# Optimization experiments

Hardware: AMD Instinct MI355X
Metric: run time of the kernel (lower is better)

Reference implementation:

```python
import jax, jax.numpy as jnp
import numpy as np

E, E2, T, C, H = 500_000, 1_000_000, 1_000_000, 64, 64
EPS, EPS2 = 0.0, 0.0  # train_eps=False, eps=eps2=0.0


def setup_inputs() -> dict:
    key = jax.random.key(0)
    ks = jax.random.split(key, 16)
    s = 1.0 / np.sqrt(C)
    return {
        "edge_attr": jax.random.normal(ks[0], (E, C), jnp.float32),
        "edge_attr2": jax.random.normal(ks[1], (E2, C), jnp.float32),
        # 6 projection layers (C -> C)
        "Wp": jax.random.normal(ks[2], (6, C, C), jnp.float32) * s,
        "bp": jnp.zeros((6, C), jnp.float32),
        # MLP 0 (for 1-hop edges): C -> H -> C
        "W1a": jax.random.normal(ks[3], (C, H), jnp.float32) * s,
        "b1a": jnp.zeros((H,), jnp.float32),
        "W2a": jax.random.normal(ks[4], (H, C), jnp.float32) * (1.0 / np.sqrt(H)),
        "b2a": jnp.zeros((C,), jnp.float32),
        # MLP 1 (for 2-hop edges): C -> H -> C
        "W1b": jax.random.normal(ks[5], (C, H), jnp.float32) * s,
        "b1b": jnp.zeros((H,), jnp.float32),
        "W2b": jax.random.normal(ks[6], (H, C), jnp.float32) * (1.0 / np.sqrt(H)),
        "b2b": jnp.zeros((C,), jnp.float32),
        # triangle index lists [3, T]; all values < E so valid for both edge arrays
        "triangle_1_1_1": jax.random.randint(ks[7], (3, T), 0, E, jnp.int64),
        "triangle_1_1_2": jax.random.randint(ks[8], (3, T), 0, E, jnp.int64),
        "triangle_1_2_2": jax.random.randint(ks[9], (3, T), 0, E, jnp.int64),
        "triangle_2_2_2": jax.random.randint(ks[10], (3, T), 0, E, jnp.int64),
        "inverse_edge_1": jax.random.randint(ks[11], (E,), 0, E, jnp.int64),
        "inverse_edge_2": jax.random.randint(ks[12], (E2,), 0, E, jnp.int64),
    }


def reference(edge_attr, edge_attr2, Wp, bp, W1a, b1a, W2a, b2a,
              W1b, b1b, W2b, b2b,
              triangle_1_1_1, triangle_1_1_2, triangle_1_2_2, triangle_2_2_2,
              inverse_edge_1, inverse_edge_2):
    num_edges = edge_attr.shape[0]
    num_edges2 = edge_attr2.shape[0]

    def proj(i, x):  # Linear proj i applied to gathered-sum features
        return x @ Wp[i] + bp[i]

    def mlp_a(x):
        return jax.nn.relu(x @ W1a + b1a) @ W2a + b2a

    def mlp_b(x):
        return jax.nn.relu(x @ W1b + b1b) @ W2b + b2b

    ij111, ik111, kj111 = triangle_1_1_1
    ij112, ik112, kj112 = triangle_1_1_2
    ij122, ik122, kj122 = triangle_1_2_2
    ij222, ik222, kj222 = triangle_2_2_2

    m111 = jax.ops.segment_sum(proj(0, edge_attr[ik111] + edge_attr[kj111]), ij111, num_segments=num_edges)
    m112 = jax.ops.segment_sum(proj(1, edge_attr[ik112] + edge_attr2[kj112]), ij112, num_segments=num_edges)
    m122 = jax.ops.segment_sum(proj(2, edge_attr2[ik122] + edge_attr2[kj122]), ij122, num_segments=num_edges)
    edge_attr = mlp_a(edge_attr * (1.0 + EPS) + m111 + m112 + m112[inverse_edge_1] + m122)

    m211 = jax.ops.segment_sum(proj(3, edge_attr[ij112] + edge_attr[ik112]), kj112, num_segments=num_edges2)
    m212 = jax.ops.segment_sum(proj(4, edge_attr[ij122] + edge_attr2[kj122]), ik122, num_segments=num_edges2)
    m222 = jax.ops.segment_sum(proj(5, edge_attr2[ik222] + edge_attr2[kj222]), ij222, num_segments=num_edges2)
    edge_attr2 = mlp_b(edge_attr2 * (1.0 + EPS2) + m211 + m212 + m212[inverse_edge_2] + m222)

    return (edge_attr, edge_attr2)
```

## Files before the change

kernel.cpp:

```cpp
#include <hip/hip_runtime.h>

#define CH 64
typedef unsigned int uint;
typedef unsigned short ushort;

typedef __attribute__((ext_vector_type(8))) short bf16x8;
typedef __attribute__((ext_vector_type(4))) float f32x4;

__device__ __forceinline__ float bf_lo(uint u){ union{uint a;float f;}c; c.a=u<<16; return c.f; }
__device__ __forceinline__ float bf_hi(uint u){ union{uint a;float f;}c; c.a=u&0xffff0000u; return c.f; }
__device__ __forceinline__ ushort f2bf(float f){
    uint a = __float_as_uint(f);
    a = (a + 0x7fffu + ((a>>16)&1u)) >> 16;
    return (ushort)a;
}
__device__ __forceinline__ uint pack2(float lo, float hi){
    return (uint)f2bf(lo) | ((uint)f2bf(hi) << 16);
}
__device__ __forceinline__ void atom_pk(uint* addr, float lo, float hi){
    uint v = pack2(lo, hi);
    asm volatile("global_atomic_pk_add_bf16 %0, %1, off" :: "v"(addr), "v"(v) : "memory");
}

template<bool ABF, bool BBF>
__global__ __launch_bounds__(256) void scatter_sum(
    const void* __restrict__ Av, const void* __restrict__ Bv,
    const int* __restrict__ idx_dst, const int* __restrict__ idx_a,
    const int* __restrict__ idx_b, int T,
    uint* __restrict__ S, float* __restrict__ cnt)
{
    const int l32  = threadIdx.x & 31;
    const int half = (threadIdx.x >> 5) & 1;
    const int wave  = blockIdx.x * (blockDim.x >> 6) + (threadIdx.x >> 6);
    const int nwave = gridDim.x * (blockDim.x >> 6);
    for (int w = wave; 2 * w < T; w += nwave) {
        const int t = 2 * w + half;
        if (t >= T) continue;
        const int ia = idx_a[t], ib = idx_b[t], id = idx_dst[t];
        float ax, ay, bx, by;
        if (ABF) { uint u = ((const uint*)Av)[(size_t)ia*32 + l32]; ax = bf_lo(u); ay = bf_hi(u); }
        else     { float2 v = ((const float2*)Av)[(size_t)ia*32 + l32]; ax = v.x; ay = v.y; }
        if (BBF) { uint u = ((const uint*)Bv)[(size_t)ib*32 + l32]; bx = bf_lo(u); by = bf_hi(u); }
        else     { float2 v = ((const float2*)Bv)[(size_t)ib*32 + l32]; bx = v.x; by = v.y; }
        atom_pk(S + (size_t)id*32 + l32, ax+bx, ay+by);
        if (l32 == 0) atomicAdd(&cnt[id], 1.0f);
    }
}

__global__ __launch_bounds__(256) void conv_bf16_kernel(
    const float* __restrict__ src, uint* __restrict__ dst, long n4)
{
    long i = (long)blockIdx.x * blockDim.x + threadIdx.x;
    const long stride = (long)gridDim.x * blockDim.x;
    for (; i < n4; i += stride) {
        const float4 v = ((const float4*)src)[i];
        uint2 o; o.x = pack2(v.x, v.y); o.y = pack2(v.z, v.w);
        ((uint2*)dst)[i] = o;
    }
}

__global__ __launch_bounds__(256) void fused_finalize_mfma(
    const float* __restrict__ base,
    const uint* __restrict__ SA, const float* __restrict__ cA,
    const float* __restrict__ WA, const float* __restrict__ bA,
    const uint* __restrict__ SB, const float* __restrict__ cB,
    const float* __restrict__ WB, const float* __restrict__ bB,
    const uint* __restrict__ SC, const float* __restrict__ cC,
    const float* __restrict__ WC, const float* __restrict__ bC,
    const int* __restrict__ inv,
    const float* __restrict__ W1, const float* __restrict__ b1,
    const float* __restrict__ W2, const float* __restrict__ b2,
    int N, float* __restrict__ out)
{
    __shared__ __attribute__((aligned(16))) char lds[49152];
    const int tid = threadIdx.x;

    const float* Wlist[5] = {WA, WB, WC, W1, W2};
    #pragma unroll
    for (int m = 0; m < 5; ++m) {
        const float* Wm = Wlist[m];
        for (int idx = tid; idx < 4096; idx += 256) {
            const int k = idx >> 6, col = idx & 63;
            *(ushort*)(lds + m*8192 + col*128 + ((2*k) ^ ((col&7)<<4))) = f2bf(Wm[idx]);
        }
    }
    __syncthreads();

    const int w = tid >> 6, lane = tid & 63;
    const int ln = lane & 15, grp = lane >> 4;
    const int r0 = blockIdx.x * 64 + w * 16;
    const int ra = (r0 + ln) < N ? (r0 + ln) : (N - 1);
    const int iva = inv[ra];
    char* zl = lds + 40960 + w * 2048;

    auto ldS = [&](const uint* Srow, int kc) {
        union { uint4 u; bf16x8 h; } c;
        c.u = *(const uint4*)(Srow + kc*16 + grp*4);
        return c.h;
    };
    auto ldS2 = [&](const uint* r1, const uint* r2, int kc) {
        const uint4 a = *(const uint4*)(r1 + kc*16 + grp*4);
        const uint4 b = *(const uint4*)(r2 + kc*16 + grp*4);
        union { uint4 u; bf16x8 h; } c;
        c.u.x = pack2(bf_lo(a.x)+bf_lo(b.x), bf_hi(a.x)+bf_hi(b.x));
        c.u.y = pack2(bf_lo(a.y)+bf_lo(b.y), bf_hi(a.y)+bf_hi(b.y));
        c.u.z = pack2(bf_lo(a.z)+bf_lo(b.z), bf_hi(a.z)+bf_hi(b.z));
        c.u.w = pack2(bf_lo(a.w)+bf_lo(b.w), bf_hi(a.w)+bf_hi(b.w));
        return c.h;
    };
    auto ldW = [&](int m, int kc, int ct) {
        const int col = ct*16 + ln;
        const int k2  = (kc*32 + grp*8) * 2;
        return *(const bf16x8*)(lds + m*8192 + col*128 + (k2 ^ ((col&7)<<4)));
    };
    auto ldZ = [&](int kc) {
        const int k2 = (kc*32 + grp*8) * 2;
        return *(const bf16x8*)(zl + ln*128 + (k2 ^ ((ln&7)<<4)));
    };
    auto stZ = [&](int row, int col, float v) {
        *(ushort*)(zl + row*128 + ((2*col) ^ ((row&7)<<4))) = f2bf(v);
    };

    const uint* SArow  = SA + (size_t)ra * 32;
    const uint* SBrow  = SB + (size_t)ra * 32;
    const uint* SCrow  = SC + (size_t)ra * 32;
    const uint* SCrow2 = SC + (size_t)iva * 32;

    const f32x4 z4 = {0.f, 0.f, 0.f, 0.f};
    f32x4 acc[4] = {z4, z4, z4, z4};

    #pragma unroll
    for (int kc = 0; kc < 2; ++kc) {
        const bf16x8 aA = ldS(SArow, kc);
        const bf16x8 aB = ldS(SBrow, kc);
        const bf16x8 aC = ldS2(SCrow, SCrow2, kc);
        #pragma unroll
        for (int ct = 0; ct < 4; ++ct) {
            acc[ct] = __builtin_amdgcn_mfma_f32_16x16x32_bf16(aA, ldW(0,kc,ct), acc[ct], 0,0,0);
            acc[ct] = __builtin_amdgcn_mfma_f32_16x16x32_bf16(aB, ldW(1,kc,ct), acc[ct], 0,0,0);
            acc[ct] = __builtin_amdgcn_mfma_f32_16x16x32_bf16(aC, ldW(2,kc,ct), acc[ct], 0,0,0);
        }
    }

    #pragma unroll
    for (int reg = 0; reg < 4; ++reg) {
        const int rd = r0 + grp*4 + reg;
        const int rc = rd < N ? rd : (N - 1);
        const float fA = cA[rc], fB = cB[rc];
        const float fC = cC[rc] + cC[inv[rc]];
        #pragma unroll
        for (int ct = 0; ct < 4; ++ct) {
            const int col = ct*16 + ln;
            acc[ct][reg] += base[(size_t)rc*64 + col] + fA*bA[col] + fB*bB[col] + fC*bC[col];
        }
    }
    #pragma unroll
    for (int ct = 0; ct < 4; ++ct)
        #pragma unroll
        for (int reg = 0; reg < 4; ++reg)
            stZ(grp*4 + reg, ct*16 + ln, acc[ct][reg]);

    f32x4 hacc[4] = {z4, z4, z4, z4};
    #pragma unroll
    for (int kc = 0; kc < 2; ++kc) {
        const bf16x8 az = ldZ(kc);
        #pragma unroll
        for (int ct = 0; ct < 4; ++ct)
            hacc[ct] = __builtin_amdgcn_mfma_f32_16x16x32_bf16(az, ldW(3,kc,ct), hacc[ct], 0,0,0);
    }
    #pragma unroll
    for (int ct = 0; ct < 4; ++ct)
        #pragma unroll
        for (int reg = 0; reg < 4; ++reg)
            stZ(grp*4 + reg, ct*16 + ln, fmaxf(hacc[ct][reg] + b1[ct*16 + ln], 0.f));

    f32x4 oacc[4] = {z4, z4, z4, z4};
    #pragma unroll
    for (int kc = 0; kc < 2; ++kc) {
        const bf16x8 ah = ldZ(kc);
        #pragma unroll
        for (int ct = 0; ct < 4; ++ct)
            oacc[ct] = __builtin_amdgcn_mfma_f32_16x16x32_bf16(ah, ldW(4,kc,ct), oacc[ct], 0,0,0);
    }
    #pragma unroll
    for (int reg = 0; reg < 4; ++reg) {
        const int rd = r0 + grp*4 + reg;
        if (rd < N) {
            #pragma unroll
            for (int ct = 0; ct < 4; ++ct) {
                const int col = ct*16 + ln;
                out[(size_t)rd*64 + col] = oacc[ct][reg] + b2[col];
            }
        }
    }
}

extern "C" void kernel_launch(void* const* d_in, const int* in_sizes, int n_in,
                              void* d_out, int out_size, void* d_ws, size_t ws_size,
                              hipStream_t stream)
{
    const float* ea  = (const float*)d_in[0];
    const float* ea2 = (const float*)d_in[1];
    const float* Wp  = (const float*)d_in[2];
    const float* bp  = (const float*)d_in[3];
    const float* W1a = (const float*)d_in[4];
    const float* b1a = (const float*)d_in[5];
    const float* W2a = (const float*)d_in[6];
    const float* b2a = (const float*)d_in[7];
    const float* W1b = (const float*)d_in[8];
    const float* b1b = (const float*)d_in[9];
    const float* W2b = (const float*)d_in[10];
    const float* b2b = (const float*)d_in[11];
    const int* t111 = (const int*)d_in[12];
    const int* t112 = (const int*)d_in[13];
    const int* t122 = (const int*)d_in[14];
    const int* t222 = (const int*)d_in[15];
    const int* inv1 = (const int*)d_in[16];
    const int* inv2 = (const int*)d_in[17];

    const int E    = in_sizes[0] / CH;
    const int E2   = in_sizes[1] / CH;
    const int T111 = in_sizes[12] / 3;
    const int T112 = in_sizes[13] / 3;
    const int T122 = in_sizes[14] / 3;
    const int T222 = in_sizes[15] / 3;

    float* out1 = (float*)d_out;
    float* out2 = out1 + (size_t)E * CH;

    const size_t R = (size_t)(E > E2 ? E : E2);
    char* p = (char*)d_ws;
    uint*  SA = (uint*)p;  p += R * 128;
    uint*  SB = (uint*)p;  p += R * 128;
    uint*  SC = (uint*)p;  p += R * 128;
    float* cA = (float*)p; p += R * 4;
    float* cB = (float*)p; p += R * 4;
    float* cC = (float*)p; p += R * 4;
    size_t used = (size_t)(p - (char*)d_ws);
    uint* ea2_bf = nullptr;
    uint* ea_bf  = nullptr;
    if (ws_size >= used + (size_t)E2 * 128) { ea2_bf = (uint*)p; p += (size_t)E2 * 128; used += (size_t)E2 * 128; }
    if (ws_size >= used + (size_t)E  * 128) { ea_bf  = (uint*)p; }

    const dim3 blk256(256);
    const int SCAT_NB = 4096;

    auto scat = [&](const void* A, bool abf, const void* B, bool bbf,
                    const int* dst, const int* ia, const int* ib, int T,
                    uint* S, float* c) {
        if (abf && bbf)
            scatter_sum<true, true ><<<SCAT_NB, blk256, 0, stream>>>(A, B, dst, ia, ib, T, S, c);
        else if (abf)
            scatter_sum<true, false><<<SCAT_NB, blk256, 0, stream>>>(A, B, dst, ia, ib, T, S, c);
        else if (bbf)
            scatter_sum<false, true><<<SCAT_NB, blk256, 0, stream>>>(A, B, dst, ia, ib, T, S, c);
        else
            scatter_sum<false, false><<<SCAT_NB, blk256, 0, stream>>>(A, B, dst, ia, ib, T, S, c);
    };

    if (ea2_bf) conv_bf16_kernel<<<2048, blk256, 0, stream>>>(ea2, ea2_bf, (long)E2 * 16);
    if (ea_bf)  conv_bf16_kernel<<<2048, blk256, 0, stream>>>(ea,  ea_bf,  (long)E  * 16);

    const void* eaS  = ea_bf  ? (const void*)ea_bf  : (const void*)ea;
    const void* ea2S = ea2_bf ? (const void*)ea2_bf : (const void*)ea2;
    const bool eaB = ea_bf != nullptr, ea2B = ea2_bf != nullptr;

    hipMemsetAsync(SA, 0, (size_t)E * 128, stream);
    hipMemsetAsync(SB, 0, (size_t)E * 128, stream);
    hipMemsetAsync(SC, 0, (size_t)E * 128, stream);
    hipMemsetAsync(cA, 0, (size_t)E * 4, stream);
    hipMemsetAsync(cB, 0, (size_t)E * 4, stream);
    hipMemsetAsync(cC, 0, (size_t)E * 4, stream);

    scat(eaS, eaB, eaS, eaB, t111 + 0, t111 + T111, t111 + 2*T111, T111, SA, cA);
    scat(ea2S, ea2B, ea2S, ea2B, t122 + 0, t122 + T122, t122 + 2*T122, T122, SB, cB);
    scat(eaS, eaB, ea2S, ea2B, t112 + 0, t112 + T112, t112 + 2*T112, T112, SC, cC);

    fused_finalize_mfma<<<(E + 63) / 64, blk256, 0, stream>>>(
        ea,
        SA, cA, Wp + 0*CH*CH, bp + 0*CH,
        SB, cB, Wp + 2*CH*CH, bp + 2*CH,
        SC, cC, Wp + 1*CH*CH, bp + 1*CH,
        inv1, W1a, b1a, W2a, b2a, E, out1);

    hipMemsetAsync(SA, 0, (size_t)E2 * 128, stream);
    hipMemsetAsync(SB, 0, (size_t)E2 * 128, stream);
    hipMemsetAsync(SC, 0, (size_t)E2 * 128, stream);
    hipMemsetAsync(cA, 0, (size_t)E2 * 4, stream);
    hipMemsetAsync(cB, 0, (size_t)E2 * 4, stream);
    hipMemsetAsync(cC, 0, (size_t)E2 * 4, stream);

    scat(out1, false, out1, false, t112 + 2*T112, t112 + 0, t112 + T112, T112, SA, cA);
    scat(ea2S, ea2B, ea2S, ea2B, t222 + 0, t222 + T222, t222 + 2*T222, T222, SB, cB);
    scat(out1, false, ea2S, ea2B, t122 + T122, t122 + 0, t122 + 2*T122, T122, SC, cC);

    fused_finalize_mfma<<<(E2 + 63) / 64, blk256, 0, stream>>>(
        ea2,
        SA, cA, Wp + 3*CH*CH, bp + 3*CH,
        SB, cB, Wp + 5*CH*CH, bp + 5*CH,
        SC, cC, Wp + 4*CH*CH, bp + 4*CH,
        inv2, W1b, b1b, W2b, b2b, E2, out2);
}
```

Measured before the change: 1.586 ms.

## Precompute bf16 weight images, loop 4 tiles per block, emit bf16 copy of layer-1 output

Adds a prep kernel that converts all ten weight matrices into swizzled bf16 LDS images once, so each finalize block just copies them instead of converting fp32 weights. Each finalize block now processes 256 rows over four 16-row tiles per wave, which amortises the weight load. The inverse-edge term is handled by an extra MFMA instead of a bf16 add, and the MFMA operands are swapped so that stores become vectorised. The finalize reads the bf16 base features, and the first stage also writes a bf16 copy of its output so the second-stage scatters gather half the bytes. In exchange, the residual base and the gathered layer-1 output now carry bf16 rounding.

```diff
diff --git a/kernel.cpp b/kernel.cpp
--- a/kernel.cpp
+++ b/kernel.cpp
@@ -59,137 +59,158 @@
     }
 }
 
+struct W10 { const float* p[10]; };
+__global__ __launch_bounds__(256) void prep_weights(W10 srcs, char* __restrict__ img)
+{
+    const float* W = srcs.p[blockIdx.x];
+    char* im = img + (size_t)blockIdx.x * 8192;
+    for (int idx = threadIdx.x; idx < 4096; idx += 256) {
+        const int k = idx >> 6, col = idx & 63;
+        *(ushort*)(im + col*128 + ((2*k) ^ ((col&7)<<4))) = f2bf(W[idx]);
+    }
+}
+
+template<bool BASEBF>
 __global__ __launch_bounds__(256) void fused_finalize_mfma(
-    const float* __restrict__ base,
+    const void* __restrict__ base,
     const uint* __restrict__ SA, const float* __restrict__ cA,
-    const float* __restrict__ WA, const float* __restrict__ bA,
     const uint* __restrict__ SB, const float* __restrict__ cB,
-    const float* __restrict__ WB, const float* __restrict__ bB,
     const uint* __restrict__ SC, const float* __restrict__ cC,
-    const float* __restrict__ WC, const float* __restrict__ bC,
     const int* __restrict__ inv,
-    const float* __restrict__ W1, const float* __restrict__ b1,
-    const float* __restrict__ W2, const float* __restrict__ b2,
-    int N, float* __restrict__ out)
+    const char* __restrict__ wi0, const char* __restrict__ wi1,
+    const char* __restrict__ wi2, const char* __restrict__ wi3,
+    const char* __restrict__ wi4,
+    const float* __restrict__ bA, const float* __restrict__ bB,
+    const float* __restrict__ bC,
+    const float* __restrict__ b1, const float* __restrict__ b2,
+    int N, float* __restrict__ out, uint* __restrict__ out_bf)
 {
     __shared__ __attribute__((aligned(16))) char lds[49152];
     const int tid = threadIdx.x;
 
-    const float* Wlist[5] = {WA, WB, WC, W1, W2};
-    #pragma unroll
-    for (int m = 0; m < 5; ++m) {
-        const float* Wm = Wlist[m];
-        for (int idx = tid; idx < 4096; idx += 256) {
-            const int k = idx >> 6, col = idx & 63;
-            *(ushort*)(lds + m*8192 + col*128 + ((2*k) ^ ((col&7)<<4))) = f2bf(Wm[idx]);
+    {
+        const char* imgs[5] = {wi0, wi1, wi2, wi3, wi4};
+        #pragma unroll
+        for (int m = 0; m < 5; ++m) {
+            const uint4* s = (const uint4*)imgs[m];
+            uint4* d = (uint4*)(lds + m*8192);
+            #pragma unroll
+            for (int i = 0; i < 2; ++i) d[tid + 256*i] = s[tid + 256*i];
         }
     }
     __syncthreads();
 
     const int w = tid >> 6, lane = tid & 63;
     const int ln = lane & 15, grp = lane >> 4;
-    const int r0 = blockIdx.x * 64 + w * 16;
-    const int ra = (r0 + ln) < N ? (r0 + ln) : (N - 1);
-    const int iva = inv[ra];
     char* zl = lds + 40960 + w * 2048;
-
+    const int swz = (ln & 7) << 4;
+
+    auto ldW = [&](int m, int kc, int ct) {
+        const int col = ct*16 + ln;
+        return *(const bf16x8*)(lds + m*8192 + col*128 + ((kc*64 + grp*16) ^ ((col&7)<<4)));
+    };
     auto ldS = [&](const uint* Srow, int kc) {
         union { uint4 u; bf16x8 h; } c;
         c.u = *(const uint4*)(Srow + kc*16 + grp*4);
         return c.h;
     };
-    auto ldS2 = [&](const uint* r1, const uint* r2, int kc) {
-        const uint4 a = *(const uint4*)(r1 + kc*16 + grp*4);
-        const uint4 b = *(const uint4*)(r2 + kc*16 + grp*4);
-        union { uint4 u; bf16x8 h; } c;
-        c.u.x = pack2(bf_lo(a.x)+bf_lo(b.x), bf_hi(a.x)+bf_hi(b.x));
-        c.u.y = pack2(bf_lo(a.y)+bf_lo(b.y), bf_hi(a.y)+bf_hi(b.y));
-        c.u.z = pack2(bf_lo(a.z)+bf_lo(b.z), bf_hi(a.z)+bf_hi(b.z));
-        c.u.w = pack2(bf_lo(a.w)+bf_lo(b.w), bf_hi(a.w)+bf_hi(b.w));
-        return c.h;
-    };
-    auto ldW = [&](int m, int kc, int ct) {
-        const int col = ct*16 + ln;
-        const int k2  = (kc*32 + grp*8) * 2;
-        return *(const bf16x8*)(lds + m*8192 + col*128 + (k2 ^ ((col&7)<<4)));
-    };
     auto ldZ = [&](int kc) {
-        const int k2 = (kc*32 + grp*8) * 2;
-        return *(const bf16x8*)(zl + ln*128 + (k2 ^ ((ln&7)<<4)));
-    };
-    auto stZ = [&](int row, int col, float v) {
-        *(ushort*)(zl + row*128 + ((2*col) ^ ((row&7)<<4))) = f2bf(v);
-    };
-
-    const uint* SArow  = SA + (size_t)ra * 32;
-    const uint* SBrow  = SB + (size_t)ra * 32;
-    const uint* SCrow  = SC + (size_t)ra * 32;
-    const uint* SCrow2 = SC + (size_t)iva * 32;
+        return *(const bf16x8*)(zl + ln*128 + ((kc*64 + grp*16) ^ swz));
+    };
+    auto stZ = [&](int ct, float v0, float v1, float v2, float v3) {
+        uint2 u; u.x = pack2(v0, v1); u.y = pack2(v2, v3);
+        *(uint2*)(zl + ln*128 + ((ct*32 + grp*8) ^ swz)) = u;
+    };
 
     const f32x4 z4 = {0.f, 0.f, 0.f, 0.f};
-    f32x4 acc[4] = {z4, z4, z4, z4};
-
-    #pragma unroll
-    for (int kc = 0; kc < 2; ++kc) {
-        const bf16x8 aA = ldS(SArow, kc);
-        const bf16x8 aB = ldS(SBrow, kc);
-        const bf16x8 aC = ldS2(SCrow, SCrow2, kc);
-        #pragma unroll
-        for (int ct = 0; ct < 4; ++ct) {
-            acc[ct] = __builtin_amdgcn_mfma_f32_16x16x32_bf16(aA, ldW(0,kc,ct), acc[ct], 0,0,0);
-            acc[ct] = __builtin_amdgcn_mfma_f32_16x16x32_bf16(aB, ldW(1,kc,ct), acc[ct], 0,0,0);
-            acc[ct] = __builtin_amdgcn_mfma_f32_16x16x32_bf16(aC, ldW(2,kc,ct), acc[ct], 0,0,0);
-        }
-    }
-
-    #pragma unroll
-    for (int reg = 0; reg < 4; ++reg) {
-        const int rd = r0 + grp*4 + reg;
-        const int rc = rd < N ? rd : (N - 1);
-        const float fA = cA[rc], fB = cB[rc];
-        const float fC = cC[rc] + cC[inv[rc]];
-        #pragma unroll
-        for (int ct = 0; ct < 4; ++ct) {
-            const int col = ct*16 + ln;
-            acc[ct][reg] += base[(size_t)rc*64 + col] + fA*bA[col] + fB*bB[col] + fC*bC[col];
-        }
-    }
-    #pragma unroll
-    for (int ct = 0; ct < 4; ++ct)
-        #pragma unroll
-        for (int reg = 0; reg < 4; ++reg)
-            stZ(grp*4 + reg, ct*16 + ln, acc[ct][reg]);
-
-    f32x4 hacc[4] = {z4, z4, z4, z4};
-    #pragma unroll
-    for (int kc = 0; kc < 2; ++kc) {
-        const bf16x8 az = ldZ(kc);
-        #pragma unroll
-        for (int ct = 0; ct < 4; ++ct)
-            hacc[ct] = __builtin_amdgcn_mfma_f32_16x16x32_bf16(az, ldW(3,kc,ct), hacc[ct], 0,0,0);
-    }
-    #pragma unroll
-    for (int ct = 0; ct < 4; ++ct)
-        #pragma unroll
-        for (int reg = 0; reg < 4; ++reg)
-            stZ(grp*4 + reg, ct*16 + ln, fmaxf(hacc[ct][reg] + b1[ct*16 + ln], 0.f));
-
-    f32x4 oacc[4] = {z4, z4, z4, z4};
-    #pragma unroll
-    for (int kc = 0; kc < 2; ++kc) {
-        const bf16x8 ah = ldZ(kc);
-        #pragma unroll
-        for (int ct = 0; ct < 4; ++ct)
-            oacc[ct] = __builtin_amdgcn_mfma_f32_16x16x32_bf16(ah, ldW(4,kc,ct), oacc[ct], 0,0,0);
-    }
-    #pragma unroll
-    for (int reg = 0; reg < 4; ++reg) {
-        const int rd = r0 + grp*4 + reg;
-        if (rd < N) {
+
+    #pragma unroll 1
+    for (int t = 0; t < 4; ++t) {
+        const int rr = blockIdx.x * 256 + w * 64 + t * 16 + ln;
+        const int ra = rr < N ? rr : N - 1;
+        const bool valid = rr < N;
+        const int iv = inv[ra];
+        const float fA = cA[ra], fB = cB[ra], fC = cC[ra] + cC[iv];
+
+        const uint* SArow  = SA + (size_t)ra * 32;
+        const uint* SBrow  = SB + (size_t)ra * 32;
+        const uint* SCrow  = SC + (size_t)ra * 32;
+        const uint* SCrow2 = SC + (size_t)iv * 32;
+
+        f32x4 acc[4] = {z4, z4, z4, z4};
+        #pragma unroll
+        for (int kc = 0; kc < 2; ++kc) {
+            const bf16x8 sA = ldS(SArow, kc);
+            const bf16x8 sB = ldS(SBrow, kc);
+            const bf16x8 sC = ldS(SCrow, kc);
+            const bf16x8 sD = ldS(SCrow2, kc);
             #pragma unroll
             for (int ct = 0; ct < 4; ++ct) {
-                const int col = ct*16 + ln;
-                out[(size_t)rd*64 + col] = oacc[ct][reg] + b2[col];
+                const bf16x8 wC = ldW(2, kc, ct);
+                acc[ct] = __builtin_amdgcn_mfma_f32_16x16x32_bf16(ldW(0,kc,ct), sA, acc[ct], 0,0,0);
+                acc[ct] = __builtin_amdgcn_mfma_f32_16x16x32_bf16(ldW(1,kc,ct), sB, acc[ct], 0,0,0);
+                acc[ct] = __builtin_amdgcn_mfma_f32_16x16x32_bf16(wC,          sC, acc[ct], 0,0,0);
+                acc[ct] = __builtin_amdgcn_mfma_f32_16x16x32_bf16(wC,          sD, acc[ct], 0,0,0);
+            }
+        }
+
+        #pragma unroll
+        for (int ct = 0; ct < 4; ++ct) {
+            const int cb = ct*16 + grp*4;
+            const float4 vA = *(const float4*)(bA + cb);
+            const float4 vB = *(const float4*)(bB + cb);
+            const float4 vC = *(const float4*)(bC + cb);
+            float e0, e1, e2, e3;
+            if (BASEBF) {
+                const uint2 u = *(const uint2*)((const uint*)base + (size_t)ra*32 + (cb>>1));
+                e0 = bf_lo(u.x); e1 = bf_hi(u.x); e2 = bf_lo(u.y); e3 = bf_hi(u.y);
+            } else {
+                const float4 b4 = *(const float4*)((const float*)base + (size_t)ra*64 + cb);
+                e0 = b4.x; e1 = b4.y; e2 = b4.z; e3 = b4.w;
+            }
+            stZ(ct,
+                acc[ct][0] + e0 + fA*vA.x + fB*vB.x + fC*vC.x,
+                acc[ct][1] + e1 + fA*vA.y + fB*vB.y + fC*vC.y,
+                acc[ct][2] + e2 + fA*vA.z + fB*vB.z + fC*vC.z,
+                acc[ct][3] + e3 + fA*vA.w + fB*vB.w + fC*vC.w);
+        }
+
+        f32x4 hacc[4] = {z4, z4, z4, z4};
+        #pragma unroll
+        for (int kc = 0; kc < 2; ++kc) {
+            const bf16x8 zf = ldZ(kc);
+            #pragma unroll
+            for (int ct = 0; ct < 4; ++ct)
+                hacc[ct] = __builtin_amdgcn_mfma_f32_16x16x32_bf16(ldW(3,kc,ct), zf, hacc[ct], 0,0,0);
+        }
+        #pragma unroll
+        for (int ct = 0; ct < 4; ++ct) {
+            const int cb = ct*16 + grp*4;
+            const float4 v1 = *(const float4*)(b1 + cb);
+            stZ(ct, fmaxf(hacc[ct][0] + v1.x, 0.f), fmaxf(hacc[ct][1] + v1.y, 0.f),
+                    fmaxf(hacc[ct][2] + v1.z, 0.f), fmaxf(hacc[ct][3] + v1.w, 0.f));
+        }
+
+        f32x4 oacc[4] = {z4, z4, z4, z4};
+        #pragma unroll
+        for (int kc = 0; kc < 2; ++kc) {
+            const bf16x8 hf = ldZ(kc);
+            #pragma unroll
+            for (int ct = 0; ct < 4; ++ct)
+                oacc[ct] = __builtin_amdgcn_mfma_f32_16x16x32_bf16(ldW(4,kc,ct), hf, oacc[ct], 0,0,0);
+        }
+        #pragma unroll
+        for (int ct = 0; ct < 4; ++ct) {
+            const int cb = ct*16 + grp*4;
+            const float4 v2 = *(const float4*)(b2 + cb);
+            const float o0 = oacc[ct][0] + v2.x, o1 = oacc[ct][1] + v2.y;
+            const float o2 = oacc[ct][2] + v2.z, o3 = oacc[ct][3] + v2.w;
+            if (valid) {
+                *(float4*)(out + (size_t)ra*64 + cb) = make_float4(o0, o1, o2, o3);
+                if (out_bf) {
+                    uint2 u; u.x = pack2(o0, o1); u.y = pack2(o2, o3);
+                    *(uint2*)(out_bf + (size_t)ra*32 + (cb>>1)) = u;
+                }
             }
         }
     }
@@ -230,6 +251,7 @@
 
     const size_t R = (size_t)(E > E2 ? E : E2);
     char* p = (char*)d_ws;
+    char*  Wimg = p;       p += 10 * 8192;
     uint*  SA = (uint*)p;  p += R * 128;
     uint*  SB = (uint*)p;  p += R * 128;
     uint*  SC = (uint*)p;  p += R * 128;
@@ -239,8 +261,10 @@
     size_t used = (size_t)(p - (char*)d_ws);
     uint* ea2_bf = nullptr;
     uint* ea_bf  = nullptr;
+    uint* out1_bf = nullptr;
     if (ws_size >= used + (size_t)E2 * 128) { ea2_bf = (uint*)p; p += (size_t)E2 * 128; used += (size_t)E2 * 128; }
-    if (ws_size >= used + (size_t)E  * 128) { ea_bf  = (uint*)p; }
+    if (ws_size >= used + (size_t)E  * 128) { ea_bf  = (uint*)p; p += (size_t)E  * 128; used += (size_t)E  * 128; }
+    if (ws_size >= used + (size_t)E  * 128) { out1_bf = (uint*)p; }
 
     const dim3 blk256(256);
     const int SCAT_NB = 4096;
@@ -258,6 +282,11 @@
             scatter_sum<false, false><<<SCAT_NB, blk256, 0, stream>>>(A, B, dst, ia, ib, T, S, c);
     };
 
+    W10 w10;
+    for (int i = 0; i < 6; ++i) w10.p[i] = Wp + (size_t)i * CH * CH;
+    w10.p[6] = W1a; w10.p[7] = W2a; w10.p[8] = W1b; w10.p[9] = W2b;
+    prep_weights<<<10, blk256, 0, stream>>>(w10, Wimg);
+
     if (ea2_bf) conv_bf16_kernel<<<2048, blk256, 0, stream>>>(ea2, ea2_bf, (long)E2 * 16);
     if (ea_bf)  conv_bf16_kernel<<<2048, blk256, 0, stream>>>(ea,  ea_bf,  (long)E  * 16);
 
@@ -276,12 +305,20 @@
     scat(ea2S, ea2B, ea2S, ea2B, t122 + 0, t122 + T122, t122 + 2*T122, T122, SB, cB);
     scat(eaS, eaB, ea2S, ea2B, t112 + 0, t112 + T112, t112 + 2*T112, T112, SC, cC);
 
-    fused_finalize_mfma<<<(E + 63) / 64, blk256, 0, stream>>>(
-        ea,
-        SA, cA, Wp + 0*CH*CH, bp + 0*CH,
-        SB, cB, Wp + 2*CH*CH, bp + 2*CH,
-        SC, cC, Wp + 1*CH*CH, bp + 1*CH,
-        inv1, W1a, b1a, W2a, b2a, E, out1);
+    {
+        const void* base1 = eaB ? (const void*)ea_bf : (const void*)ea;
+        const int NB = (E + 255) / 256;
+        if (eaB)
+            fused_finalize_mfma<true><<<NB, blk256, 0, stream>>>(
+                base1, SA, cA, SB, cB, SC, cC, inv1,
+                Wimg + 0*8192, Wimg + 2*8192, Wimg + 1*8192, Wimg + 6*8192, Wimg + 7*8192,
+                bp + 0*CH, bp + 2*CH, bp + 1*CH, b1a, b2a, E, out1, out1_bf);
+        else
+            fused_finalize_mfma<false><<<NB, blk256, 0, stream>>>(
+                base1, SA, cA, SB, cB, SC, cC, inv1,
+                Wimg + 0*8192, Wimg + 2*8192, Wimg + 1*8192, Wimg + 6*8192, Wimg + 7*8192,
+                bp + 0*CH, bp + 2*CH, bp + 1*CH, b1a, b2a, E, out1, out1_bf);
+    }
 
     hipMemsetAsync(SA, 0, (size_t)E2 * 128, stream);
     hipMemsetAsync(SB, 0, (size_t)E2 * 128, stream);
@@ -290,14 +327,25 @@
     hipMemsetAsync(cB, 0, (size_t)E2 * 4, stream);
     hipMemsetAsync(cC, 0, (size_t)E2 * 4, stream);
 
-    scat(out1, false, out1, false, t112 + 2*T112, t112 + 0, t112 + T112, T112, SA, cA);
+    const void* o1S = out1_bf ? (const void*)out1_bf : (const void*)out1;
+    const bool o1B = out1_bf != nullptr;
+
+    scat(o1S, o1B, o1S, o1B, t112 + 2*T112, t112 + 0, t112 + T112, T112, SA, cA);
     scat(ea2S, ea2B, ea2S, ea2B, t222 + 0, t222 + T222, t222 + 2*T222, T222, SB, cB);
-    scat(out1, false, ea2S, ea2B, t122 + T122, t122 + 0, t122 + 2*T122, T122, SC, cC);
-
-    fused_finalize_mfma<<<(E2 + 63) / 64, blk256, 0, stream>>>(
-        ea2,
-        SA, cA, Wp + 3*CH*CH, bp + 3*CH,
-        SB, cB, Wp + 5*CH*CH, bp + 5*CH,
-        SC, cC, Wp + 4*CH*CH, bp + 4*CH,
-        inv2, W1b, b1b, W2b, b2b, E2, out2);
-}
+    scat(o1S, o1B, ea2S, ea2B, t122 + T122, t122 + 0, t122 + 2*T122, T122, SC, cC);
+
+    {
+        const void* base2 = ea2B ? (const void*)ea2_bf : (const void*)ea2;
+        const int NB = (E2 + 255) / 256;
+        if (ea2B)
+            fused_finalize_mfma<true><<<NB, blk256, 0, stream>>>(
+                base2, SA, cA, SB, cB, SC, cC, inv2,
+                Wimg + 3*8192, Wimg + 5*8192, Wimg + 4*8192, Wimg + 8*8192, Wimg + 9*8192,
+                bp + 3*CH, bp + 5*CH, bp + 4*CH, b1b, b2b, E2, out2, nullptr);
+        else
+            fused_finalize_mfma<false><<<NB, blk256, 0, stream>>>(
+                base2, SA, cA, SB, cB, SC, cC, inv2,
+                Wimg + 3*8192, Wimg + 5*8192, Wimg + 4*8192, Wimg + 8*8192, Wimg + 9*8192,
+                bp + 3*CH, bp + 5*CH, bp + 4*CH, b1b, b2b, E2, out2, nullptr);
+    }
+}
```

After: 1.765 ms. 11.3% more time.

## Precompute bf16 weight images, emit bf16 out1 copy, read bf16 base in finalize

Applied to the files above, without the earlier changes.

Adds a one-time prep kernel that converts all ten weight matrices into the swizzled bf16 LDS layout, so each finalize block copies them with vector loads instead of converting from fp32. The first finalize also writes a bf16 copy of out1, which the second-stage scatters gather instead of fp32 rows, halving their gather traffic. Finalize reads the residual base from the bf16 copies when available. Trade-offs: extra workspace, an extra bf16 store per output element, and reduced precision in the residual term and in the second-stage gathers.

```diff
diff --git a/kernel.cpp b/kernel.cpp
--- a/kernel.cpp
+++ b/kernel.cpp
@@ -59,29 +59,43 @@
     }
 }
 
+struct W10 { const float* p[10]; };
+__global__ __launch_bounds__(256) void prep_weights(W10 srcs, char* __restrict__ img)
+{
+    const float* W = srcs.p[blockIdx.x];
+    char* im = img + (size_t)blockIdx.x * 8192;
+    for (int idx = threadIdx.x; idx < 4096; idx += 256) {
+        const int k = idx >> 6, col = idx & 63;
+        *(ushort*)(im + col*128 + ((2*k) ^ ((col&7)<<4))) = f2bf(W[idx]);
+    }
+}
+
+template<bool BASEBF>
 __global__ __launch_bounds__(256) void fused_finalize_mfma(
-    const float* __restrict__ base,
+    const void* __restrict__ base,
     const uint* __restrict__ SA, const float* __restrict__ cA,
-    const float* __restrict__ WA, const float* __restrict__ bA,
     const uint* __restrict__ SB, const float* __restrict__ cB,
-    const float* __restrict__ WB, const float* __restrict__ bB,
     const uint* __restrict__ SC, const float* __restrict__ cC,
-    const float* __restrict__ WC, const float* __restrict__ bC,
     const int* __restrict__ inv,
-    const float* __restrict__ W1, const float* __restrict__ b1,
-    const float* __restrict__ W2, const float* __restrict__ b2,
-    int N, float* __restrict__ out)
+    const char* __restrict__ wiA, const char* __restrict__ wiB,
+    const char* __restrict__ wiC, const char* __restrict__ wi1,
+    const char* __restrict__ wi2,
+    const float* __restrict__ bA, const float* __restrict__ bB,
+    const float* __restrict__ bC,
+    const float* __restrict__ b1, const float* __restrict__ b2,
+    int N, float* __restrict__ out, uint* __restrict__ out_bf)
 {
     __shared__ __attribute__((aligned(16))) char lds[49152];
     const int tid = threadIdx.x;
 
-    const float* Wlist[5] = {WA, WB, WC, W1, W2};
-    #pragma unroll
-    for (int m = 0; m < 5; ++m) {
-        const float* Wm = Wlist[m];
-        for (int idx = tid; idx < 4096; idx += 256) {
-            const int k = idx >> 6, col = idx & 63;
-            *(ushort*)(lds + m*8192 + col*128 + ((2*k) ^ ((col&7)<<4))) = f2bf(Wm[idx]);
+    {
+        const char* imgs[5] = {wiA, wiB, wiC, wi1, wi2};
+        #pragma unroll
+        for (int m = 0; m < 5; ++m) {
+            const uint4* s = (const uint4*)imgs[m];
+            uint4* d = (uint4*)(lds + m*8192);
+            #pragma unroll
+            for (int i = 0; i < 2; ++i) d[tid + 256*i] = s[tid + 256*i];
         }
     }
     __syncthreads();
@@ -151,7 +165,14 @@
         #pragma unroll
         for (int ct = 0; ct < 4; ++ct) {
             const int col = ct*16 + ln;
-            acc[ct][reg] += base[(size_t)rc*64 + col] + fA*bA[col] + fB*bB[col] + fC*bC[col];
+            float e;
+            if (BASEBF) {
+                const uint u = ((const uint*)base)[(size_t)rc*32 + (col>>1)];
+                e = (col & 1) ? bf_hi(u) : bf_lo(u);
+            } else {
+                e = ((const float*)base)[(size_t)rc*64 + col];
+            }
+            acc[ct][reg] += e + fA*bA[col] + fB*bB[col] + fC*bC[col];
         }
     }
     #pragma unroll
@@ -189,7 +210,9 @@
             #pragma unroll
             for (int ct = 0; ct < 4; ++ct) {
                 const int col = ct*16 + ln;
-                out[(size_t)rd*64 + col] = oacc[ct][reg] + b2[col];
+                const float o = oacc[ct][reg] + b2[col];
+                out[(size_t)rd*64 + col] = o;
+                if (out_bf) ((ushort*)out_bf)[(size_t)rd*64 + col] = f2bf(o);
             }
         }
     }
@@ -230,6 +253,7 @@
 
     const size_t R = (size_t)(E > E2 ? E : E2);
     char* p = (char*)d_ws;
+    char*  Wimg = p;       p += 10 * 8192;
     uint*  SA = (uint*)p;  p += R * 128;
     uint*  SB = (uint*)p;  p += R * 128;
     uint*  SC = (uint*)p;  p += R * 128;
@@ -238,8 +262,10 @@
     float* cC = (float*)p; p += R * 4;
     size_t used = (size_t)(p - (char*)d_ws);
     uint* ea2_bf = nullptr;
+    uint* out1_bf = nullptr;
     uint* ea_bf  = nullptr;
     if (ws_size >= used + (size_t)E2 * 128) { ea2_bf = (uint*)p; p += (size_t)E2 * 128; used += (size_t)E2 * 128; }
+    if (ws_size >= used + (size_t)E  * 128) { out1_bf = (uint*)p; p += (size_t)E * 128; used += (size_t)E * 128; }
     if (ws_size >= used + (size_t)E  * 128) { ea_bf  = (uint*)p; }
 
     const dim3 blk256(256);
@@ -258,6 +284,11 @@
             scatter_sum<false, false><<<SCAT_NB, blk256, 0, stream>>>(A, B, dst, ia, ib, T, S, c);
     };
 
+    W10 w10;
+    for (int i = 0; i < 6; ++i) w10.p[i] = Wp + (size_t)i * CH * CH;
+    w10.p[6] = W1a; w10.p[7] = W2a; w10.p[8] = W1b; w10.p[9] = W2b;
+    prep_weights<<<10, blk256, 0, stream>>>(w10, Wimg);
+
     if (ea2_bf) conv_bf16_kernel<<<2048, blk256, 0, stream>>>(ea2, ea2_bf, (long)E2 * 16);
     if (ea_bf)  conv_bf16_kernel<<<2048, blk256, 0, stream>>>(ea,  ea_bf,  (long)E  * 16);
 
@@ -276,12 +307,19 @@
     scat(ea2S, ea2B, ea2S, ea2B, t122 + 0, t122 + T122, t122 + 2*T122, T122, SB, cB);
     scat(eaS, eaB, ea2S, ea2B, t112 + 0, t112 + T112, t112 + 2*T112, T112, SC, cC);
 
-    fused_finalize_mfma<<<(E + 63) / 64, blk256, 0, stream>>>(
-        ea,
-        SA, cA, Wp + 0*CH*CH, bp + 0*CH,
-        SB, cB, Wp + 2*CH*CH, bp + 2*CH,
-        SC, cC, Wp + 1*CH*CH, bp + 1*CH,
-        inv1, W1a, b1a, W2a, b2a, E, out1);
+    {
+        const int NB = (E + 63) / 64;
+        if (eaB)
+            fused_finalize_mfma<true><<<NB, blk256, 0, stream>>>(
+                (const void*)ea_bf, SA, cA, SB, cB, SC, cC, inv1,
+                Wimg + 0*8192, Wimg + 2*8192, Wimg + 1*8192, Wimg + 6*8192, Wimg + 7*8192,
+                bp + 0*CH, bp + 2*CH, bp + 1*CH, b1a, b2a, E, out1, out1_bf);
+        else
+            fused_finalize_mfma<false><<<NB, blk256, 0, stream>>>(
+                (const void*)ea, SA, cA, SB, cB, SC, cC, inv1,
+                Wimg + 0*8192, Wimg + 2*8192, Wimg + 1*8192, Wimg + 6*8192, Wimg + 7*8192,
+                bp + 0*CH, bp + 2*CH, bp + 1*CH, b1a, b2a, E, out1, out1_bf);
+    }
 
     hipMemsetAsync(SA, 0, (size_t)E2 * 128, stream);
     hipMemsetAsync(SB, 0, (size_t)E2 * 128, stream);
@@ -290,14 +328,24 @@
     hipMemsetAsync(cB, 0, (size_t)E2 * 4, stream);
     hipMemsetAsync(cC, 0, (size_t)E2 * 4, stream);
 
-    scat(out1, false, out1, false, t112 + 2*T112, t112 + 0, t112 + T112, T112, SA, cA);
+    const void* o1S = out1_bf ? (const void*)out1_bf : (const void*)out1;
+    const bool o1B = out1_bf != nullptr;
+
+    scat(o1S, o1B, o1S, o1B, t112 + 2*T112, t112 + 0, t112 + T112, T112, SA, cA);
     scat(ea2S, ea2B, ea2S, ea2B, t222 + 0, t222 + T222, t222 + 2*T222, T222, SB, cB);
-    scat(out1, false, ea2S, ea2B, t122 + T122, t122 + 0, t122 + 2*T122, T122, SC, cC);
-
-    fused_finalize_mfma<<<(E2 + 63) / 64, blk256, 0, stream>>>(
-        ea2,
-        SA, cA, Wp + 3*CH*CH, bp + 3*CH,
-        SB, cB, Wp + 5*CH*CH, bp + 5*CH,
-        SC, cC, Wp + 4*CH*CH, bp + 4*CH,
-        inv2, W1b, b1b, W2b, b2b, E2, out2);
-}
+    scat(o1S, o1B, ea2S, ea2B, t122 + T122, t122 + 0, t122 + 2*T122, T122, SC, cC);
+
+    {
+        const int NB = (E2 + 63) / 64;
+        if (ea2B)
+            fused_finalize_mfma<true><<<NB, blk256, 0, stream>>>(
+                (const void*)ea2_bf, SA, cA, SB, cB, SC, cC, inv2,
+                Wimg + 3*8192, Wimg + 5*8192, Wimg + 4*8192, Wimg + 8*8192, Wimg + 9*8192,
+                bp + 3*CH, bp + 5*CH, bp + 4*CH, b1b, b2b, E2, out2, nullptr);
+        else
+            fused_finalize_mfma<false><<<NB, blk256, 0, stream>>>(
+                (const void*)ea2, SA, cA, SB, cB, SC, cC, inv2,
+                Wimg + 3*8192, Wimg + 5*8192, Wimg + 4*8192, Wimg + 8*8192, Wimg + 9*8192,
+                bp + 3*CH, bp + 5*CH, bp + 4*CH, b1b, b2b, E2, out2, nullptr);
+    }
+}
```

After: 1.786 ms. 12.6% more time.

## Emit bf16 copy of layer-1 output and unroll scatter to two triangles per half-wave

Applied to the files above, without the earlier changes.

The first fused finalize kernel now also writes a bf16 copy of its output into workspace, and the second-stage scatters gather from that copy instead of fp32, halving gather bytes. The scatter loop handles two triangles per half-wave with all loads issued before the atomics, which raises memory-level parallelism. The memory clobber on the packed bf16 atomic asm is removed so the compiler can reorder around it. In exchange there is an extra bf16 write in finalize, more workspace use, and a small precision loss on the gathered layer-1 features.

```diff
diff --git a/kernel.cpp b/kernel.cpp
--- a/kernel.cpp
+++ b/kernel.cpp
@@ -19,7 +19,7 @@
 }
 __device__ __forceinline__ void atom_pk(uint* addr, float lo, float hi){
     uint v = pack2(lo, hi);
-    asm volatile("global_atomic_pk_add_bf16 %0, %1, off" :: "v"(addr), "v"(v) : "memory");
+    asm volatile("global_atomic_pk_add_bf16 %0, %1, off" :: "v"(addr), "v"(v));
 }
 
 template<bool ABF, bool BBF>
@@ -33,17 +33,34 @@
     const int half = (threadIdx.x >> 5) & 1;
     const int wave  = blockIdx.x * (blockDim.x >> 6) + (threadIdx.x >> 6);
     const int nwave = gridDim.x * (blockDim.x >> 6);
-    for (int w = wave; 2 * w < T; w += nwave) {
-        const int t = 2 * w + half;
-        if (t >= T) continue;
-        const int ia = idx_a[t], ib = idx_b[t], id = idx_dst[t];
-        float ax, ay, bx, by;
-        if (ABF) { uint u = ((const uint*)Av)[(size_t)ia*32 + l32]; ax = bf_lo(u); ay = bf_hi(u); }
-        else     { float2 v = ((const float2*)Av)[(size_t)ia*32 + l32]; ax = v.x; ay = v.y; }
-        if (BBF) { uint u = ((const uint*)Bv)[(size_t)ib*32 + l32]; bx = bf_lo(u); by = bf_hi(u); }
-        else     { float2 v = ((const float2*)Bv)[(size_t)ib*32 + l32]; bx = v.x; by = v.y; }
-        atom_pk(S + (size_t)id*32 + l32, ax+bx, ay+by);
-        if (l32 == 0) atomicAdd(&cnt[id], 1.0f);
+
+    for (int w = wave; 4 * w < T; w += nwave) {
+        const int t0 = 4 * w + half;
+        const int t1 = t0 + 2;
+        const bool v0 = t0 < T, v1 = t1 < T;
+        const int u0 = v0 ? t0 : 0;
+        const int u1 = v1 ? t1 : 0;
+        const int ia0 = idx_a[u0], ib0 = idx_b[u0], id0 = idx_dst[u0];
+        const int ia1 = idx_a[u1], ib1 = idx_b[u1], id1 = idx_dst[u1];
+
+        float ax0, ay0, bx0, by0, ax1, ay1, bx1, by1;
+        if (ABF) { uint u = ((const uint*)Av)[(size_t)ia0*32 + l32]; ax0 = bf_lo(u); ay0 = bf_hi(u); }
+        else     { float2 v = ((const float2*)Av)[(size_t)ia0*32 + l32]; ax0 = v.x; ay0 = v.y; }
+        if (BBF) { uint u = ((const uint*)Bv)[(size_t)ib0*32 + l32]; bx0 = bf_lo(u); by0 = bf_hi(u); }
+        else     { float2 v = ((const float2*)Bv)[(size_t)ib0*32 + l32]; bx0 = v.x; by0 = v.y; }
+        if (ABF) { uint u = ((const uint*)Av)[(size_t)ia1*32 + l32]; ax1 = bf_lo(u); ay1 = bf_hi(u); }
+        else     { float2 v = ((const float2*)Av)[(size_t)ia1*32 + l32]; ax1 = v.x; ay1 = v.y; }
+        if (BBF) { uint u = ((const uint*)Bv)[(size_t)ib1*32 + l32]; bx1 = bf_lo(u); by1 = bf_hi(u); }
+        else     { float2 v = ((const float2*)Bv)[(size_t)ib1*32 + l32]; bx1 = v.x; by1 = v.y; }
+
+        if (v0) {
+            atom_pk(S + (size_t)id0*32 + l32, ax0+bx0, ay0+by0);
+            if (l32 == 0) atomicAdd(&cnt[id0], 1.0f);
+        }
+        if (v1) {
+            atom_pk(S + (size_t)id1*32 + l32, ax1+bx1, ay1+by1);
+            if (l32 == 0) atomicAdd(&cnt[id1], 1.0f);
+        }
     }
 }
 
@@ -70,7 +87,7 @@
     const int* __restrict__ inv,
     const float* __restrict__ W1, const float* __restrict__ b1,
     const float* __restrict__ W2, const float* __restrict__ b2,
-    int N, float* __restrict__ out)
+    int N, float* __restrict__ out, uint* __restrict__ out_bf)
 {
     __shared__ __attribute__((aligned(16))) char lds[49152];
     const int tid = threadIdx.x;
@@ -189,7 +206,9 @@
             #pragma unroll
             for (int ct = 0; ct < 4; ++ct) {
                 const int col = ct*16 + ln;
-                out[(size_t)rd*64 + col] = oacc[ct][reg] + b2[col];
+                const float o = oacc[ct][reg] + b2[col];
+                out[(size_t)rd*64 + col] = o;
+                if (out_bf) ((ushort*)out_bf)[(size_t)rd*64 + col] = f2bf(o);
             }
         }
     }
@@ -238,8 +257,10 @@
     float* cC = (float*)p; p += R * 4;
     size_t used = (size_t)(p - (char*)d_ws);
     uint* ea2_bf = nullptr;
+    uint* out1_bf = nullptr;
     uint* ea_bf  = nullptr;
     if (ws_size >= used + (size_t)E2 * 128) { ea2_bf = (uint*)p; p += (size_t)E2 * 128; used += (size_t)E2 * 128; }
+    if (ws_size >= used + (size_t)E  * 128) { out1_bf = (uint*)p; p += (size_t)E * 128; used += (size_t)E * 128; }
     if (ws_size >= used + (size_t)E  * 128) { ea_bf  = (uint*)p; }
 
     const dim3 blk256(256);
@@ -281,7 +302,7 @@
         SA, cA, Wp + 0*CH*CH, bp + 0*CH,
         SB, cB, Wp + 2*CH*CH, bp + 2*CH,
         SC, cC, Wp + 1*CH*CH, bp + 1*CH,
-        inv1, W1a, b1a, W2a, b2a, E, out1);
+        inv1, W1a, b1a, W2a, b2a, E, out1, out1_bf);
 
     hipMemsetAsync(SA, 0, (size_t)E2 * 128, stream);
     hipMemsetAsync(SB, 0, (size_t)E2 * 128, stream);
@@ -290,14 +311,17 @@
     hipMemsetAsync(cB, 0, (size_t)E2 * 4, stream);
     hipMemsetAsync(cC, 0, (size_t)E2 * 4, stream);
 
-    scat(out1, false, out1, false, t112 + 2*T112, t112 + 0, t112 + T112, T112, SA, cA);
+    const void* o1S = out1_bf ? (const void*)out1_bf : (const void*)out1;
+    const bool o1B = out1_bf != nullptr;
+
+    scat(o1S, o1B, o1S, o1B, t112 + 2*T112, t112 + 0, t112 + T112, T112, SA, cA);
     scat(ea2S, ea2B, ea2S, ea2B, t222 + 0, t222 + T222, t222 + 2*T222, T222, SB, cB);
-    scat(out1, false, ea2S, ea2B, t122 + T122, t122 + 0, t122 + 2*T122, T122, SC, cC);
+    scat(o1S, o1B, ea2S, ea2B, t122 + T122, t122 + 0, t122 + 2*T122, T122, SC, cC);
 
     fused_finalize_mfma<<<(E2 + 63) / 64, blk256, 0, stream>>>(
         ea2,
         SA, cA, Wp + 3*CH*CH, bp + 3*CH,
         SB, cB, Wp + 5*CH*CH, bp + 5*CH,
         SC, cC, Wp + 4*CH*CH, bp + 4*CH,
-        inv2, W1b, b1b, W2b, b2b, E2, out2);
-}
+        inv2, W1b, b1b, W2b, b2b, E2, out2, nullptr);
+}
```

After: 1.642 ms. 1.04x slower.
